# Optimization experiments

Hardware: AMD Instinct MI355X
Metric: run time of the kernel (lower is better)

## Reference

```python
import jax, jax.numpy as jnp
import numpy as np

EMBED_DIM = 512
NUM_HEADS = 8
HEAD_DIM = EMBED_DIM // NUM_HEADS
EDGE_DIM = 16
B, N = 2, 2048


def setup_inputs() -> dict:
    key = jax.random.key(0)
    ks = jax.random.split(key, 16)
    s = 1.0 / np.sqrt(EMBED_DIM)
    inp = {
        "x": jax.random.normal(ks[0], (B, N, EMBED_DIM), dtype=jnp.float32),
        "adjacency": jax.random.uniform(ks[1], (B, N, N), dtype=jnp.float32),
        # torch.nn.Linear stores weight as (out, in); we keep that convention
        "Wq": jax.random.uniform(ks[2], (EMBED_DIM, EMBED_DIM), minval=-s, maxval=s),
        "bq": jax.random.uniform(ks[3], (EMBED_DIM,), minval=-s, maxval=s),
        "Wk": jax.random.uniform(ks[4], (EMBED_DIM, EMBED_DIM), minval=-s, maxval=s),
        "bk": jax.random.uniform(ks[5], (EMBED_DIM,), minval=-s, maxval=s),
        "Wv": jax.random.uniform(ks[6], (EMBED_DIM, EMBED_DIM), minval=-s, maxval=s),
        "bv": jax.random.uniform(ks[7], (EMBED_DIM,), minval=-s, maxval=s),
        "Wo": jax.random.uniform(ks[8], (EMBED_DIM, EMBED_DIM), minval=-s, maxval=s),
        "bo": jax.random.uniform(ks[9], (EMBED_DIM,), minval=-s, maxval=s),
        # edge MLP: Linear(1 -> edge_dim) then Linear(edge_dim -> num_heads)
        "We1": jax.random.uniform(ks[10], (EDGE_DIM, 1), minval=-1.0, maxval=1.0),
        "be1": jax.random.uniform(ks[11], (EDGE_DIM,), minval=-1.0, maxval=1.0),
        "We2": jax.random.uniform(ks[12], (NUM_HEADS, EDGE_DIM), minval=-0.25, maxval=0.25),
        "be2": jax.random.uniform(ks[13], (NUM_HEADS,), minval=-0.25, maxval=0.25),
        "edge_bias": jnp.zeros((NUM_HEADS,), dtype=jnp.float32),
    }
    return inp


def reference(x, adjacency, Wq, bq, Wk, bk, Wv, bv, Wo, bo, We1, be1, We2, be2, edge_bias):
    b, n, _ = x.shape
    scale = HEAD_DIM ** (-0.5)

    def split_heads(t):  # (b, n, E) -> (b, H, n, d)
        return t.reshape(b, n, NUM_HEADS, HEAD_DIM).transpose(0, 2, 1, 3)

    q = split_heads(x @ Wq.T + bq)
    k = split_heads(x @ Wk.T + bk)
    v = split_heads(x @ Wv.T + bv)

    # (b, H, n, n)
    attn_scores = jnp.einsum('bhid,bhjd->bhij', q, k) * scale

    # edge MLP applied pointwise to each adjacency entry: 1 -> edge_dim -> num_heads
    # hidden: (b, n, n, edge_dim)
    hidden = jax.nn.relu(adjacency[..., None] * We1[:, 0] + be1)
    edge_attn = jnp.einsum('bijE,hE->bhij', hidden, We2) + be2[None, :, None, None]

    boost = adjacency[:, None, :, :] * edge_bias[None, :, None, None]
    attn_scores = attn_scores + edge_attn + boost

    attn_probs = jax.nn.softmax(attn_scores, axis=-1)
    out = jnp.einsum('bhij,bhjd->bhid', attn_probs, v)
    out = out.transpose(0, 2, 1, 3).reshape(b, n, EMBED_DIM)
    out = out @ Wo.T + bo
    return out
```

## Files before the change

### kernel.cpp

```cpp
#include <hip/hip_runtime.h>
#include <stdint.h>


#define SEQ 2048
#define EMB 512
#define NH  8
#define HD  64
#define NB  2
#define L2E 1.4426950408889634f

typedef unsigned int   u32;
typedef unsigned short u16;
typedef u32   u32x4  __attribute__((ext_vector_type(4)));
typedef float f32x4  __attribute__((ext_vector_type(4)));
typedef __bf16 bf16x8 __attribute__((ext_vector_type(8)));

#define MFMA16(a, b, c) __builtin_amdgcn_mfma_f32_16x16x32_bf16((a), (b), (c), 0, 0, 0)

static __device__ __forceinline__ u16 f2bf(float f) {
  return __builtin_bit_cast(u16, (__bf16)f);
}
static __device__ __forceinline__ u32 pack2(float a, float b) {
  return (u32)f2bf(a) | ((u32)f2bf(b) << 16);
}
static __device__ __forceinline__ bf16x8 ldfrag(const u16* p) {
  return __builtin_bit_cast(bf16x8, *(const u32x4*)p);
}


__global__ void prep_kernel(const float* __restrict__ x,
                            const float* __restrict__ Wq, const float* __restrict__ Wk,
                            const float* __restrict__ Wv, const float* __restrict__ Wo,
                            const float* __restrict__ We1, const float* __restrict__ be1,
                            const float* __restrict__ We2, const float* __restrict__ be2,
                            const float* __restrict__ ebias,
                            u16* __restrict__ xb, u16* __restrict__ wqkv,
                            u16* __restrict__ wob, float* __restrict__ co) {
  const int blk = blockIdx.x, tid = threadIdx.x;
  if (blk < 2048) {
    int i = (blk * 256 + tid) * 4;
    float4 v = *(const float4*)(x + i);
    *(uint2*)(xb + i) = make_uint2(pack2(v.x, v.y), pack2(v.z, v.w));
  } else if (blk < 3072) {
    int i = ((blk - 2048) * 256 + tid) * 4;
    int m = i >> 18;
    int off = i & 262143;
    const float* src = (m == 0) ? Wq : ((m == 1) ? Wk : ((m == 2) ? Wv : Wo));
    u16* dst = (m < 3) ? (wqkv + (size_t)m * 262144) : wob;
    float4 v = *(const float4*)(src + off);
    *(uint2*)(dst + off) = make_uint2(pack2(v.x, v.y), pack2(v.z, v.w));
  } else {
    const int e = tid & 15, h = tid >> 4;
    if (tid < 128) {
      co[49 + e * 8 + h] = 0.0f;
      if (h == 0) { co[17 + e] = 0.0f; co[33 + e] = 0.0f; }
    }
    __syncthreads();
    if (tid < 128) {
      float w1 = We1[e], b1 = be1[e], w2 = We2[h * 16 + e];
      float u0 = b1, u1 = w1 + b1;
      bool on  = (u0 >= 0.0f) && (u1 >= 0.0f);
      bool off = (u0 <= 0.0f) && (u1 <= 0.0f);
      bool crossing = (!on) && (!off);
      float ca = on ? (w2 * b1) : (crossing ? 0.5f * w2 * b1 : 0.0f);
      float cb = on ? (w2 * w1) : (crossing ? 0.5f * w2 * w1 : 0.0f);
      #pragma unroll
      for (int d = 1; d < 16; d <<= 1) { ca += __shfl_xor(ca, d); cb += __shfl_xor(cb, d); }
      if (e == 0) { co[h] = (be2[h] + ca) * L2E; co[8 + h] = (ebias[h] + cb) * L2E; }
      unsigned long long msk = __ballot(crossing);
      int midx = __popcll(msk & 0xFFFFull & ((1ull << e) - 1ull));
      int mcnt = __popcll(msk & 0xFFFFull);
      if (crossing) {
        co[49 + midx * 8 + h] = 0.5f * w2 * L2E;
        if (h == 0) { co[17 + midx] = w1; co[33 + midx] = b1; }
      }
      if (tid == 0) ((int*)co)[16] = mcnt;
    }
  }
}

#define LDA 40
__global__ __launch_bounds__(256) void gemm_qkv_kernel(
    const u16* __restrict__ A, const u16* __restrict__ Bm,
    const float* __restrict__ bq, const float* __restrict__ bk, const float* __restrict__ bv,
    u16* __restrict__ qh, u16* __restrict__ ksw, u16* __restrict__ vsw)
{
  __shared__ u16 sm[64 * LDA + 128 * LDA];
  u16* As = sm;
  u16* Bs = sm + 64 * LDA;
  const int tid = threadIdx.x;
  const int lane = tid & 63, w = tid >> 6;
  const int q = lane >> 4, l15 = lane & 15;
  const int m0 = blockIdx.y * 64;
  const int n0 = blockIdx.x * 128;

  f32x4 acc[4][2];
  f32x4 zero = {0.f, 0.f, 0.f, 0.f};
  #pragma unroll
  for (int i = 0; i < 4; i++) { acc[i][0] = zero; acc[i][1] = zero; }

  const bool isA = tid < 128;
  const int arow_ = tid >> 1, ahalf = tid & 1;
  const int brow = tid - 128;
  const u16* ga = A  + (size_t)(m0 + arow_) * EMB + ahalf * 16;
  const u16* gb = Bm + (size_t)(n0 + brow) * EMB;
  u16* la = &As[arow_ * LDA + ahalf * 16];
  u16* lb = &Bs[brow * LDA];

  u32x4 p0, p1, p2, p3;
  if (isA) {
    p0 = *(const u32x4*)(ga); p1 = *(const u32x4*)(ga + 8); ga += 32;
  } else {
    p0 = *(const u32x4*)(gb);      p1 = *(const u32x4*)(gb + 8);
    p2 = *(const u32x4*)(gb + 16); p3 = *(const u32x4*)(gb + 24); gb += 32;
  }

  for (int k0 = 0; k0 < EMB; k0 += 32) {
    __syncthreads();
    if (isA) { *(u32x4*)(la) = p0; *(u32x4*)(la + 8) = p1; }
    else {
      *(u32x4*)(lb)      = p0; *(u32x4*)(lb + 8)  = p1;
      *(u32x4*)(lb + 16) = p2; *(u32x4*)(lb + 24) = p3;
    }
    __syncthreads();
    if (k0 + 32 < EMB) {
      if (isA) { p0 = *(const u32x4*)(ga); p1 = *(const u32x4*)(ga + 8); ga += 32; }
      else {
        p0 = *(const u32x4*)(gb);      p1 = *(const u32x4*)(gb + 8);
        p2 = *(const u32x4*)(gb + 16); p3 = *(const u32x4*)(gb + 24); gb += 32;
      }
    }
    bf16x8 af[4], bfr[2];
    #pragma unroll
    for (int mi = 0; mi < 4; mi++)
      af[mi] = ldfrag(&As[(mi*16 + l15) * LDA + q*8]);
    #pragma unroll
    for (int ni = 0; ni < 2; ni++)
      bfr[ni] = ldfrag(&Bs[(w*32 + ni*16 + l15) * LDA + q*8]);
    #pragma unroll
    for (int mi = 0; mi < 4; mi++)
      #pragma unroll
      for (int ni = 0; ni < 2; ni++)
        acc[mi][ni] = MFMA16(af[mi], bfr[ni], acc[mi][ni]);
  }

  const int mat = n0 >> 9;
  const float* bias = (mat == 0) ? bq : ((mat == 1) ? bk : bv);
  const float mul = (mat == 0) ? 0.125f * L2E : 1.0f;
  const int b_ = m0 >> 11;
  const int nbase = m0 & 2047;

  #pragma unroll
  for (int p = 0; p < 2; p++) {
    __syncthreads();
    if ((w >> 1) == p) {
      #pragma unroll
      for (int ni = 0; ni < 2; ni++) {
        const int dd = (w & 1) * 32 + ni * 16 + l15;
        const float bsv = bias[(n0 & 511) + (w * 32 + ni * 16 + l15)];
        #pragma unroll
        for (int mi = 0; mi < 4; mi++) {
          #pragma unroll
          for (int r = 0; r < 4; r++) {
            const int nr = mi * 16 + q * 4 + r;
            const float val = (acc[mi][ni][r] + bsv) * mul;
            int idx;
            if (mat == 0)      idx = nr * 64 + dd;
            else if (mat == 1) idx = (nr >> 4) * 1024 + ((dd >> 5) << 9)
                                   + ((((dd >> 3) & 3) * 16 + (nr & 15)) << 3) + (dd & 7);
            else               idx = ((dd >> 4) << 10) + (((nr >> 5) & 1) << 9)
                                   + ((((nr >> 3) & 3) * 16 + (dd & 15)) << 3) + (nr & 7);
            sm[idx] = f2bf(val);
          }
        }
      }
    }
    __syncthreads();
    const int hh = ((n0 & 511) >> 6) + p;
    u16* gdst;
    if (mat == 0)      gdst = qh  + ((size_t)(b_ * NH + hh) * SEQ + nbase) * HD;
    else if (mat == 1) gdst = ksw + (size_t)(b_ * NH + hh) * 131072 + (nbase >> 4) * 1024;
    else               gdst = vsw + (size_t)(b_ * NH + hh) * 131072 + (nbase >> 6) * 4096;
    *(u32x4*)(gdst + tid * 16)     = *(const u32x4*)(sm + tid * 16);
    *(u32x4*)(gdst + tid * 16 + 8) = *(const u32x4*)(sm + tid * 16 + 8);
  }
}

__global__ __launch_bounds__(256) void gemm_out_kernel(
    const u16* __restrict__ A, const u16* __restrict__ Bm,
    const float* __restrict__ bo, float* __restrict__ out)
{
  __shared__ u16 As[64 * LDA];
  __shared__ u16 Bs[64 * LDA];
  const int tid = threadIdx.x;
  const int lane = tid & 63, w = tid >> 6;
  const int q = lane >> 4, l15 = lane & 15;
  const int m0 = blockIdx.y * 64;
  const int n0 = blockIdx.x * 64;

  f32x4 acc[4];
  f32x4 zero = {0.f, 0.f, 0.f, 0.f};
  #pragma unroll
  for (int i = 0; i < 4; i++) acc[i] = zero;

  const bool isA = tid < 128;
  const int row = isA ? (tid >> 1) : ((tid - 128) >> 1);
  const int half = tid & 1;
  const u16* g = (isA ? A + (size_t)(m0 + row) * EMB : Bm + (size_t)(n0 + row) * EMB)
               + half * 16;
  u16* l = (isA ? &As[row * LDA] : &Bs[row * LDA]) + half * 16;

  u32x4 p0 = *(const u32x4*)(g);
  u32x4 p1 = *(const u32x4*)(g + 8);
  g += 32;

  for (int k0 = 0; k0 < EMB; k0 += 32) {
    __syncthreads();
    *(u32x4*)(l) = p0; *(u32x4*)(l + 8) = p1;
    __syncthreads();
    if (k0 + 32 < EMB) {
      p0 = *(const u32x4*)(g); p1 = *(const u32x4*)(g + 8); g += 32;
    }
    bf16x8 af[4], bfr;
    #pragma unroll
    for (int mi = 0; mi < 4; mi++)
      af[mi] = ldfrag(&As[(mi*16 + l15) * LDA + q*8]);
    bfr = ldfrag(&Bs[(w*16 + l15) * LDA + q*8]);
    #pragma unroll
    for (int mi = 0; mi < 4; mi++)
      acc[mi] = MFMA16(af[mi], bfr, acc[mi]);
  }

  int col = n0 + w*16 + l15;
  float bsv = bo[col];
  #pragma unroll
  for (int mi = 0; mi < 4; mi++) {
    int rowb = m0 + mi*16 + q*4;
    #pragma unroll
    for (int r = 0; r < 4; r++)
      out[(size_t)(rowb + r) * EMB + col] = acc[mi][r] + bsv;
  }
}

template<int MT>
__device__ __forceinline__ void flash_body(
    u16* __restrict__ smem,
    const u16* __restrict__ qh, const u16* __restrict__ ksw, const u16* __restrict__ vsw,
    const float* __restrict__ adj, const float* __restrict__ coeff, u16* __restrict__ om)
{
  const int tid = threadIdx.x, lane = tid & 63, w = tid >> 6;
  const int q = lane >> 4, l15 = lane & 15;
  const int i0 = blockIdx.x * 64;
  const int h = blockIdx.y, b = blockIdx.z;
  const int bh = b * NH + h;
  const int iw = i0 + w * 16;

  const float Ah = coeff[h], Bh = coeff[8 + h];
  float ctr[MT], dtr[MT], wtr[MT];
  #pragma unroll
  for (int t = 0; t < MT; t++) {
    ctr[t] = coeff[17 + t];
    dtr[t] = coeff[33 + t];
    wtr[t] = coeff[49 + t * 8 + h];
  }

  const u16* qrow = qh + ((size_t)bh * SEQ + iw + l15) * HD;
  bf16x8 qf0 = ldfrag(qrow + q * 8);
  bf16x8 qf1 = ldfrag(qrow + 32 + q * 8);

  const u16* kbase = ksw + (size_t)bh * 131072 + lane * 8;
  const u16* vbase = vsw + (size_t)bh * 131072 + lane * 8;
  const float* arow = adj + ((size_t)b * SEQ + iw + l15) * SEQ + q * 4;

  f32x4 O[4];
  f32x4 zero = {0.f, 0.f, 0.f, 0.f};
  #pragma unroll
  for (int dt = 0; dt < 4; dt++) O[dt] = zero;
  float lsum = 0.0f;

  u16* psw = smem + w * 16 * 72;

  bf16x8 kf[8];
  float4 av[4];
  #pragma unroll
  for (int jt = 0; jt < 4; jt++) {
    kf[jt*2]   = ldfrag(kbase + jt * 1024);
    kf[jt*2+1] = ldfrag(kbase + jt * 1024 + 512);
    av[jt] = *(const float4*)(arow + jt * 16);
  }

  #pragma unroll 1
  for (int it = 0; it < 32; it++) {
    const int off = it * 4096;
    const int nx = (it + 1 < 32) ? it + 1 : 31;
    const int noff = nx * 4096;

    bf16x8 vf[8];
    #pragma unroll
    for (int dt = 0; dt < 2; dt++) {
      vf[dt*2]   = ldfrag(vbase + off + dt * 1024);
      vf[dt*2+1] = ldfrag(vbase + off + dt * 1024 + 512);
    }

    f32x4 S[4];
    #pragma unroll
    for (int jt = 0; jt < 4; jt++) {
      f32x4 s = MFMA16(kf[jt*2], qf0, zero);
      S[jt] = MFMA16(kf[jt*2+1], qf1, s);
    }

    #pragma unroll
    for (int jt = 0; jt < 4; jt++) {
      kf[jt*2]   = ldfrag(kbase + noff + jt * 1024);
      kf[jt*2+1] = ldfrag(kbase + noff + jt * 1024 + 512);
    }
    #pragma unroll
    for (int dt = 2; dt < 4; dt++) {
      vf[dt*2]   = ldfrag(vbase + off + dt * 1024);
      vf[dt*2+1] = ldfrag(vbase + off + dt * 1024 + 512);
    }

    #pragma unroll
    for (int jt = 0; jt < 4; jt++) {
      float p[4];
      #pragma unroll
      for (int r = 0; r < 4; r++) {
        float a = ((const float*)&av[jt])[r];
        float e = fmaf(a, Bh, Ah);
        #pragma unroll
        for (int t = 0; t < MT; t++)
          e = fmaf(fabsf(fmaf(a, ctr[t], dtr[t])), wtr[t], e);
        p[r] = __builtin_amdgcn_exp2f(S[jt][r] + e);
        lsum += p[r];
      }
      av[jt] = *(const float4*)(arow + nx * 64 + jt * 16);
      *(uint2*)(psw + l15 * 72 + jt * 16 + q * 4) =
          make_uint2(pack2(p[0], p[1]), pack2(p[2], p[3]));
    }

    bf16x8 pf0 = ldfrag(psw + l15 * 72 + q * 8);
    bf16x8 pf1 = ldfrag(psw + l15 * 72 + 32 + q * 8);
    #pragma unroll
    for (int dt = 0; dt < 4; dt++) {
      O[dt] = MFMA16(vf[dt*2],   pf0, O[dt]);
      O[dt] = MFMA16(vf[dt*2+1], pf1, O[dt]);
    }
  }

  lsum += __shfl_xor(lsum, 16);
  lsum += __shfl_xor(lsum, 32);
  float rl = 1.0f / lsum;

  u16* orow = om + ((size_t)b * SEQ + iw + l15) * EMB + h * HD + q * 4;
  #pragma unroll
  for (int dt = 0; dt < 4; dt++) {
    float v0 = O[dt][0] * rl, v1 = O[dt][1] * rl;
    float v2 = O[dt][2] * rl, v3 = O[dt][3] * rl;
    *(uint2*)(orow + dt * 16) = make_uint2(pack2(v0, v1), pack2(v2, v3));
  }
}

__global__ __launch_bounds__(256, 3) void flash_kernel(
    const u16* __restrict__ qh, const u16* __restrict__ ksw, const u16* __restrict__ vsw,
    const float* __restrict__ adj, const float* __restrict__ coeff, u16* __restrict__ om)
{
  __shared__ __align__(16) u16 smem[4 * 16 * 72];
  const int mt = ((const int*)coeff)[16];
  if (mt <= 4)      flash_body<4>(smem, qh, ksw, vsw, adj, coeff, om);
  else if (mt <= 8) flash_body<8>(smem, qh, ksw, vsw, adj, coeff, om);
  else              flash_body<16>(smem, qh, ksw, vsw, adj, coeff, om);
}

extern "C" void kernel_launch(void* const* d_in, const int* in_sizes, int n_in,
                              void* d_out, int out_size, void* d_ws, size_t ws_size,
                              hipStream_t stream) {
  const float* x     = (const float*)d_in[0];
  const float* adj   = (const float*)d_in[1];
  const float* Wq    = (const float*)d_in[2];
  const float* bq    = (const float*)d_in[3];
  const float* Wk    = (const float*)d_in[4];
  const float* bk    = (const float*)d_in[5];
  const float* Wv    = (const float*)d_in[6];
  const float* bv    = (const float*)d_in[7];
  const float* Wo    = (const float*)d_in[8];
  const float* bo    = (const float*)d_in[9];
  const float* We1   = (const float*)d_in[10];
  const float* be1   = (const float*)d_in[11];
  const float* We2   = (const float*)d_in[12];
  const float* be2   = (const float*)d_in[13];
  const float* ebias = (const float*)d_in[14];
  float* out = (float*)d_out;

  char* ws = (char*)d_ws;
  u16*   xb   = (u16*)(ws + 0);
  u16*   wqkv = (u16*)(ws + 4194304);
  u16*   wob  = (u16*)(ws + 5767168);
  u16*   qh   = (u16*)(ws + 6291456);
  u16*   ksw  = (u16*)(ws + 10485760);
  u16*   vsw  = (u16*)(ws + 14680064);
  u16*   om   = (u16*)(ws + 18874368);
  float* co   = (float*)(ws + 23068672);
  if (ws_size < 23069696) return;

  prep_kernel<<<3073, 256, 0, stream>>>(x, Wq, Wk, Wv, Wo, We1, be1, We2, be2, ebias,
                                        xb, wqkv, wob, co);
  gemm_qkv_kernel<<<dim3(12, 64), 256, 0, stream>>>(xb, wqkv, bq, bk, bv, qh, ksw, vsw);
  flash_kernel<<<dim3(32, NH, NB), 256, 0, stream>>>(qh, ksw, vsw, adj, co, om);
  gemm_out_kernel<<<dim3(8, 64), 256, 0, stream>>>(om, wob, bo, out);
}
```

Measured before the change: 201.0 us.

## Stage K/V tiles through double-buffered LDS with async global_load_lds

```diff
diff --git a/kernel.cpp b/kernel.cpp
--- a/kernel.cpp
+++ b/kernel.cpp
@@ -25,6 +25,11 @@
 }
 static __device__ __forceinline__ bf16x8 ldfrag(const u16* p) {
   return __builtin_bit_cast(bf16x8, *(const u32x4*)p);
+}
+static __device__ __forceinline__ void glds16(const u16* g, u16* l) {
+  __builtin_amdgcn_global_load_lds(
+      (const __attribute__((address_space(1))) u32*)(const void*)g,
+      (__attribute__((address_space(3))) u32*)(void*)l, 16, 0, 0);
 }
 
 
@@ -243,8 +248,83 @@
 }
 
 template<int MT>
+struct FlashCtx {
+  const u16 *kgp, *vgp;
+  const float* arow;
+  bf16x8 qf0, qf1;
+  float Ah, Bh;
+  float ctr[MT], dtr[MT], wtr[MT];
+  int lane, w, q, l15;
+};
+
+template<int MT>
+static __device__ __forceinline__ void flash_stage(const FlashCtx<MT>& c,
+                                                   u16* Kb, u16* Vb, int it) {
+  const int o = c.w * 1024 + c.lane * 8;
+  const u16* kg = c.kgp + it * 4096;
+  const u16* vg = c.vgp + it * 4096;
+  glds16(kg + o,       Kb + o);
+  glds16(kg + o + 512, Kb + o + 512);
+  glds16(vg + o,       Vb + o);
+  glds16(vg + o + 512, Vb + o + 512);
+}
+
+template<int MT>
+static __device__ __forceinline__ void flash_iter(
+    const FlashCtx<MT>& c, int it, u16* Kb, u16* Vb, u16* nKb, u16* nVb,
+    u16* psw, float4* avc, float4* avn, f32x4* O, float& lsum)
+{
+  __syncthreads();
+  if (it + 1 < 32) flash_stage(c, nKb, nVb, it + 1);
+  const int nx = (it + 1 < 32) ? it + 1 : 31;
+  #pragma unroll
+  for (int jt = 0; jt < 4; jt++)
+    avn[jt] = *(const float4*)(c.arow + nx * 64 + jt * 16);
+  __builtin_amdgcn_sched_barrier(0);
+
+  f32x4 zero = {0.f, 0.f, 0.f, 0.f};
+  const int lo = c.lane * 8;
+
+  f32x4 S[4];
+  #pragma unroll
+  for (int jt = 0; jt < 4; jt++) {
+    bf16x8 kf0 = ldfrag(Kb + jt * 1024 + lo);
+    bf16x8 kf1 = ldfrag(Kb + jt * 1024 + 512 + lo);
+    f32x4 s = MFMA16(kf0, c.qf0, zero);
+    S[jt] = MFMA16(kf1, c.qf1, s);
+  }
+
+  #pragma unroll
+  for (int half = 0; half < 2; half++) {
+    #pragma unroll
+    for (int jj = 0; jj < 2; jj++) {
+      const int jt = half * 2 + jj;
+      float p[4];
+      #pragma unroll
+      for (int r = 0; r < 4; r++) {
+        float a = ((const float*)&avc[jt])[r];
+        float e = fmaf(a, c.Bh, c.Ah);
+        #pragma unroll
+        for (int t = 0; t < MT; t++)
+          e = fmaf(fabsf(fmaf(a, c.ctr[t], c.dtr[t])), c.wtr[t], e);
+        p[r] = __builtin_amdgcn_exp2f(S[jt][r] + e);
+        lsum += p[r];
+      }
+      *(uint2*)(psw + c.l15 * 72 + jt * 16 + c.q * 4) =
+          make_uint2(pack2(p[0], p[1]), pack2(p[2], p[3]));
+    }
+    bf16x8 pf = ldfrag(psw + c.l15 * 72 + half * 32 + c.q * 8);
+    #pragma unroll
+    for (int dt = 0; dt < 4; dt++) {
+      bf16x8 vf = ldfrag(Vb + dt * 1024 + half * 512 + lo);
+      O[dt] = MFMA16(vf, pf, O[dt]);
+    }
+  }
+}
+
+template<int MT>
 __device__ __forceinline__ void flash_body(
-    u16* __restrict__ smem,
+    u16* Kb0, u16* Kb1, u16* Vb0, u16* Vb1, u16* Pb,
     const u16* __restrict__ qh, const u16* __restrict__ ksw, const u16* __restrict__ vsw,
     const float* __restrict__ adj, const float* __restrict__ coeff, u16* __restrict__ om)
 {
@@ -255,22 +335,21 @@
   const int bh = b * NH + h;
   const int iw = i0 + w * 16;
 
-  const float Ah = coeff[h], Bh = coeff[8 + h];
-  float ctr[MT], dtr[MT], wtr[MT];
+  FlashCtx<MT> c;
+  c.lane = lane; c.w = w; c.q = q; c.l15 = l15;
+  c.Ah = coeff[h]; c.Bh = coeff[8 + h];
   #pragma unroll
   for (int t = 0; t < MT; t++) {
-    ctr[t] = coeff[17 + t];
-    dtr[t] = coeff[33 + t];
-    wtr[t] = coeff[49 + t * 8 + h];
-  }
-
+    c.ctr[t] = coeff[17 + t];
+    c.dtr[t] = coeff[33 + t];
+    c.wtr[t] = coeff[49 + t * 8 + h];
+  }
   const u16* qrow = qh + ((size_t)bh * SEQ + iw + l15) * HD;
-  bf16x8 qf0 = ldfrag(qrow + q * 8);
-  bf16x8 qf1 = ldfrag(qrow + 32 + q * 8);
-
-  const u16* kbase = ksw + (size_t)bh * 131072 + lane * 8;
-  const u16* vbase = vsw + (size_t)bh * 131072 + lane * 8;
-  const float* arow = adj + ((size_t)b * SEQ + iw + l15) * SEQ + q * 4;
+  c.qf0 = ldfrag(qrow + q * 8);
+  c.qf1 = ldfrag(qrow + 32 + q * 8);
+  c.kgp = ksw + (size_t)bh * 131072;
+  c.vgp = vsw + (size_t)bh * 131072;
+  c.arow = adj + ((size_t)b * SEQ + iw + l15) * SEQ + q * 4;
 
   f32x4 O[4];
   f32x4 zero = {0.f, 0.f, 0.f, 0.f};
@@ -278,73 +357,18 @@
   for (int dt = 0; dt < 4; dt++) O[dt] = zero;
   float lsum = 0.0f;
 
-  u16* psw = smem + w * 16 * 72;
-
-  bf16x8 kf[8];
-  float4 av[4];
-  #pragma unroll
-  for (int jt = 0; jt < 4; jt++) {
-    kf[jt*2]   = ldfrag(kbase + jt * 1024);
-    kf[jt*2+1] = ldfrag(kbase + jt * 1024 + 512);
-    av[jt] = *(const float4*)(arow + jt * 16);
-  }
+  u16* psw = Pb + w * 1152;
+
+  flash_stage(c, Kb0, Vb0, 0);
+  float4 avA[4], avB[4];
+  #pragma unroll
+  for (int jt = 0; jt < 4; jt++)
+    avA[jt] = *(const float4*)(c.arow + jt * 16);
 
   #pragma unroll 1
-  for (int it = 0; it < 32; it++) {
-    const int off = it * 4096;
-    const int nx = (it + 1 < 32) ? it + 1 : 31;
-    const int noff = nx * 4096;
-
-    bf16x8 vf[8];
-    #pragma unroll
-    for (int dt = 0; dt < 2; dt++) {
-      vf[dt*2]   = ldfrag(vbase + off + dt * 1024);
-      vf[dt*2+1] = ldfrag(vbase + off + dt * 1024 + 512);
-    }
-
-    f32x4 S[4];
-    #pragma unroll
-    for (int jt = 0; jt < 4; jt++) {
-      f32x4 s = MFMA16(kf[jt*2], qf0, zero);
-      S[jt] = MFMA16(kf[jt*2+1], qf1, s);
-    }
-
-    #pragma unroll
-    for (int jt = 0; jt < 4; jt++) {
-      kf[jt*2]   = ldfrag(kbase + noff + jt * 1024);
-      kf[jt*2+1] = ldfrag(kbase + noff + jt * 1024 + 512);
-    }
-    #pragma unroll
-    for (int dt = 2; dt < 4; dt++) {
-      vf[dt*2]   = ldfrag(vbase + off + dt * 1024);
-      vf[dt*2+1] = ldfrag(vbase + off + dt * 1024 + 512);
-    }
-
-    #pragma unroll
-    for (int jt = 0; jt < 4; jt++) {
-      float p[4];
-      #pragma unroll
-      for (int r = 0; r < 4; r++) {
-        float a = ((const float*)&av[jt])[r];
-        float e = fmaf(a, Bh, Ah);
-        #pragma unroll
-        for (int t = 0; t < MT; t++)
-          e = fmaf(fabsf(fmaf(a, ctr[t], dtr[t])), wtr[t], e);
-        p[r] = __builtin_amdgcn_exp2f(S[jt][r] + e);
-        lsum += p[r];
-      }
-      av[jt] = *(const float4*)(arow + nx * 64 + jt * 16);
-      *(uint2*)(psw + l15 * 72 + jt * 16 + q * 4) =
-          make_uint2(pack2(p[0], p[1]), pack2(p[2], p[3]));
-    }
-
-    bf16x8 pf0 = ldfrag(psw + l15 * 72 + q * 8);
-    bf16x8 pf1 = ldfrag(psw + l15 * 72 + 32 + q * 8);
-    #pragma unroll
-    for (int dt = 0; dt < 4; dt++) {
-      O[dt] = MFMA16(vf[dt*2],   pf0, O[dt]);
-      O[dt] = MFMA16(vf[dt*2+1], pf1, O[dt]);
-    }
+  for (int it2 = 0; it2 < 32; it2 += 2) {
+    flash_iter(c, it2,     Kb0, Vb0, Kb1, Vb1, psw, avA, avB, O, lsum);
+    flash_iter(c, it2 + 1, Kb1, Vb1, Kb0, Vb0, psw, avB, avA, O, lsum);
   }
 
   lsum += __shfl_xor(lsum, 16);
@@ -364,11 +388,16 @@
     const u16* __restrict__ qh, const u16* __restrict__ ksw, const u16* __restrict__ vsw,
     const float* __restrict__ adj, const float* __restrict__ coeff, u16* __restrict__ om)
 {
-  __shared__ __align__(16) u16 smem[4 * 16 * 72];
+  __shared__ __align__(16) u16 Kb[2][4096];
+  __shared__ __align__(16) u16 Vb[2][4096];
+  __shared__ __align__(16) u16 Pb[4608];
   const int mt = ((const int*)coeff)[16];
-  if (mt <= 4)      flash_body<4>(smem, qh, ksw, vsw, adj, coeff, om);
-  else if (mt <= 8) flash_body<8>(smem, qh, ksw, vsw, adj, coeff, om);
-  else              flash_body<16>(smem, qh, ksw, vsw, adj, coeff, om);
+  if (mt <= 4)
+    flash_body<4>(Kb[0], Kb[1], Vb[0], Vb[1], Pb, qh, ksw, vsw, adj, coeff, om);
+  else if (mt <= 8)
+    flash_body<8>(Kb[0], Kb[1], Vb[0], Vb[1], Pb, qh, ksw, vsw, adj, coeff, om);
+  else
+    flash_body<16>(Kb[0], Kb[1], Vb[0], Vb[1], Pb, qh, ksw, vsw, adj, coeff, om);
 }
 
 extern "C" void kernel_launch(void* const* d_in, const int* in_sizes, int n_in,
```

After: 193.3 us. 3.9% less time.
